# Kernel tuning notes

Hardware: AMD Instinct MI355X
Metric: run time of the kernel (lower is better)

The kernel has to match this reference:

```python
import jax, jax.numpy as jnp
import numpy as np

FEAT = 256
HID = 256
HEADS = 4
DH = HID // HEADS
SCALE = DH ** (-0.5)


def _linear(x, W, b):
    # torch nn.Linear convention: W is [out, in]
    return jnp.einsum('...i,oi->...o', x, W) + b


def _layernorm(x, gamma, beta, eps=1e-5):
    mu = jnp.mean(x, axis=-1, keepdims=True)
    var = jnp.mean(jnp.square(x - mu), axis=-1, keepdims=True)
    return (x - mu) * jax.lax.rsqrt(var + eps) * gamma + beta


def setup_inputs() -> dict:
    key = jax.random.key(0)
    ks = jax.random.split(key, 16)
    B, N = 4, 2048
    def w(k, shape, fan_in):
        return jax.random.uniform(k, shape, jnp.float32, -1.0, 1.0) / np.sqrt(fan_in)
    return {
        'x0': jax.random.normal(ks[0], (B, N, FEAT), jnp.float32),
        'x1': jax.random.normal(ks[1], (B, N, FEAT), jnp.float32),
        'Wqk': w(ks[2], (HID, FEAT), FEAT), 'bqk': w(ks[3], (HID,), FEAT),
        'Wv': w(ks[4], (HID, FEAT), FEAT), 'bv': w(ks[5], (HID,), FEAT),
        'Wp': w(ks[6], (HID, HID), HID), 'bp': w(ks[7], (HID,), HID),
        'W1': w(ks[8], (FEAT * 2, FEAT + HID), FEAT + HID), 'b1': w(ks[9], (FEAT * 2,), FEAT + HID),
        'gamma': jnp.ones((FEAT * 2,), jnp.float32), 'beta': jnp.zeros((FEAT * 2,), jnp.float32),
        'W2': w(ks[10], (FEAT, FEAT * 2), FEAT * 2), 'b2': w(ks[11], (FEAT,), FEAT * 2),
    }


def _forward(x0, x1, Wqk, bqk, Wv, bv, Wp, bp, W1, b1, gamma, beta, W2, b2):
    B, N0, _ = x0.shape
    N1 = x1.shape[1]

    def heads(t):  # [B, N, HID] -> [B, H, N, DH]
        return t.reshape(t.shape[0], t.shape[1], HEADS, DH).transpose(0, 2, 1, 3)

    qk0 = heads(_linear(x0, Wqk, bqk)) * (SCALE ** 0.5)
    qk1 = heads(_linear(x1, Wqk, bqk)) * (SCALE ** 0.5)
    v0 = heads(_linear(x0, Wv, bv))
    v1 = heads(_linear(x1, Wv, bv))

    sim = jnp.einsum('bhid,bhjd->bhij', qk0, qk1)  # [B,H,N0,N1]
    attn01 = jax.nn.softmax(sim, axis=-1)                      # rows over N1
    attn10 = jax.nn.softmax(sim.transpose(0, 1, 3, 2), axis=-1)  # [B,H,N1,N0], rows over N0

    m0 = jnp.einsum('bhij,bhjd->bhid', attn01, v1)  # [B,H,N0,DH]
    m1 = jnp.einsum('bhij,bhjd->bhid', attn10, v0)  # [B,H,N1,DH]

    def merge(t):  # [B,H,N,DH] -> [B,N,HID]
        return t.transpose(0, 2, 1, 3).reshape(t.shape[0], t.shape[2], HID)

    m0 = _linear(merge(m0), Wp, bp)
    m1 = _linear(merge(m1), Wp, bp)

    def mlp(x, m):
        h = _linear(jnp.concatenate([x, m], axis=-1), W1, b1)
        h = jax.nn.gelu(_layernorm(h, gamma, beta), approximate=False)
        return x + _linear(h, W2, b2)

    return mlp(x0, m0), mlp(x1, m1)


def reference(x0, x1, Wqk, bqk, Wv, bv, Wp, bp, W1, b1, gamma, beta, W2, b2):
    return _forward(x0, x1, Wqk, bqk, Wv, bv, Wp, bp, W1, b1, gamma, beta, W2, b2)
```

## Files before the change

### kernel.cpp

```cpp
#include <hip/hip_runtime.h>
#include <hip/hip_bf16.h>
#include <math.h>

typedef __hip_bfloat16 hbf;
typedef __attribute__((ext_vector_type(8))) short short8;
typedef __attribute__((ext_vector_type(4))) short short4v;
typedef __attribute__((ext_vector_type(4))) float f32x4;

#define ROWS 8192
#define SQSL 0.4246609001440095f

__device__ __forceinline__ short f2b(float f) {
    union { hbf h; short s; } u; u.h = __float2bfloat16(f); return u.s;
}
__device__ __forceinline__ float b2f(short s) {
    union { unsigned u; float f; } x;
    x.u = ((unsigned)(unsigned short)s) << 16; return x.f;
}

__global__ __launch_bounds__(256)
void prep(const float* __restrict__ Wqk, const float* __restrict__ Wv,
          const float* __restrict__ Wp, const float* __restrict__ W1,
          const float* __restrict__ W2,
          const float* __restrict__ bp, const float* __restrict__ b1,
          short* __restrict__ wq, short* __restrict__ wv,
          short* __restrict__ w1c, short* __restrict__ w2,
          float* __restrict__ bc)
{
    const int bid = blockIdx.x, tid = threadIdx.x;
    if (bid < 512) {
        const float* src; short* dst; int base; float sc = 1.f;
        if (bid < 64)       { src = Wqk; dst = wq; base = bid;       sc = SQSL; }
        else if (bid < 128) { src = Wv;  dst = wv; base = bid - 64; }
        else if (bid < 384) {
            int i = (bid - 128) * 256 + tid;
            int n = i >> 7, c = (i & 127) * 4;
            if (c < 256) {
                float4 f = ((const float4*)W1)[i];
                short4v s;
                s[0] = f2b(f.x); s[1] = f2b(f.y); s[2] = f2b(f.z); s[3] = f2b(f.w);
                *(short4v*)(w1c + (size_t)n * 512 + c) = s;
            }
            return;
        }
        else                { src = W2;  dst = w2; base = bid - 384; }
        int i = base * 256 + tid;
        float4 f = ((const float4*)src)[i];
        short4v s;
        s[0] = f2b(f.x * sc); s[1] = f2b(f.y * sc);
        s[2] = f2b(f.z * sc); s[3] = f2b(f.w * sc);
        *(short4v*)(dst + (size_t)i * 4) = s;
    } else if (bid < 1024) {
        int n = bid - 512;
        const float* wrow = W1 + (size_t)n * 512 + 256;
        float acc = 0.f;
        for (int k = 0; k < 256; ++k)
            acc += wrow[k] * Wp[(size_t)k * 256 + tid];
        w1c[(size_t)n * 512 + 256 + tid] = f2b(acc);
    } else {
        int n = (bid - 1024) * 256 + tid;
        const float* wrow = W1 + (size_t)n * 512 + 256;
        float acc = b1[n];
        for (int k = 0; k < 256; ++k) acc += wrow[k] * bp[k];
        bc[n] = acc;
    }
}

__global__ __launch_bounds__(256)
void gemm_qkv(const float* __restrict__ x0, const float* __restrict__ x1,
              const short* __restrict__ Wa, const short* __restrict__ Wb,
              const float* __restrict__ bias0, const float* __restrict__ bias1,
              short* __restrict__ qkb, short* __restrict__ vtb)
{
    const int fid  = blockIdx.x + (blockIdx.y << 2);
    const int col0 = (fid >> 8) * 128;
    const int row0 = (fid & 255) * 64;
    const int tid = threadIdx.x;
    const int lane = tid & 63, wave = tid >> 6;
    const int ln = lane & 15, quad = lane >> 4;
    const int wm = wave & 1, wn = wave >> 1;

    __shared__ short smem[64 * 72 + 128 * 72];
    short* As = smem;
    short* Bs = smem + 64 * 72;
    short* Vt = smem;

    const int ar = tid >> 2, ac = tid & 3;

    f32x4 acc[2][4];
    #pragma unroll
    for (int i = 0; i < 2; ++i)
        #pragma unroll
        for (int j = 0; j < 4; ++j) acc[i][j] = {0.f, 0.f, 0.f, 0.f};

    const short* wbase = (col0 < 256) ? Wa + (size_t)col0 * 256
                                      : Wb + (size_t)(col0 - 256) * 256;
    const float* xrow = (row0 + ar < ROWS)
        ? x0 + (size_t)(row0 + ar) * 256
        : x1 + (size_t)(row0 + ar - ROWS) * 256;

    float4 aF[4];
    short8 bR[4];
    #pragma unroll
    for (int i = 0; i < 4; ++i) aF[i] = ((const float4*)(xrow + ac * 16))[i];
    bR[0] = *(const short8*)(wbase + (size_t)ar * 256 + ac * 16);
    bR[1] = *(const short8*)(wbase + (size_t)ar * 256 + ac * 16 + 8);
    bR[2] = *(const short8*)(wbase + (size_t)(ar + 64) * 256 + ac * 16);
    bR[3] = *(const short8*)(wbase + (size_t)(ar + 64) * 256 + ac * 16 + 8);

    for (int k0 = 0; k0 < 256; k0 += 64) {
        {
            short8 s0, s1;
            s0[0] = f2b(aF[0].x); s0[1] = f2b(aF[0].y); s0[2] = f2b(aF[0].z); s0[3] = f2b(aF[0].w);
            s0[4] = f2b(aF[1].x); s0[5] = f2b(aF[1].y); s0[6] = f2b(aF[1].z); s0[7] = f2b(aF[1].w);
            s1[0] = f2b(aF[2].x); s1[1] = f2b(aF[2].y); s1[2] = f2b(aF[2].z); s1[3] = f2b(aF[2].w);
            s1[4] = f2b(aF[3].x); s1[5] = f2b(aF[3].y); s1[6] = f2b(aF[3].z); s1[7] = f2b(aF[3].w);
            *(short8*)&As[ar * 72 + ac * 16]     = s0;
            *(short8*)&As[ar * 72 + ac * 16 + 8] = s1;
        }
        *(short8*)&Bs[ar * 72 + ac * 16]            = bR[0];
        *(short8*)&Bs[ar * 72 + ac * 16 + 8]        = bR[1];
        *(short8*)&Bs[(ar + 64) * 72 + ac * 16]     = bR[2];
        *(short8*)&Bs[(ar + 64) * 72 + ac * 16 + 8] = bR[3];
        __syncthreads();

        if (k0 + 64 < 256) {
            const int kk = k0 + 64 + ac * 16;
            #pragma unroll
            for (int i = 0; i < 4; ++i) aF[i] = ((const float4*)(xrow + kk))[i];
            bR[0] = *(const short8*)(wbase + (size_t)ar * 256 + kk);
            bR[1] = *(const short8*)(wbase + (size_t)ar * 256 + kk + 8);
            bR[2] = *(const short8*)(wbase + (size_t)(ar + 64) * 256 + kk);
            bR[3] = *(const short8*)(wbase + (size_t)(ar + 64) * 256 + kk + 8);
        }

        short8 a[2][2], b[4][2];
        #pragma unroll
        for (int mi = 0; mi < 2; ++mi)
            #pragma unroll
            for (int ks = 0; ks < 2; ++ks)
                a[mi][ks] = *(const short8*)&As[(wm * 32 + mi * 16 + ln) * 72 + ks * 32 + quad * 8];
        #pragma unroll
        for (int nj = 0; nj < 4; ++nj)
            #pragma unroll
            for (int ks = 0; ks < 2; ++ks)
                b[nj][ks] = *(const short8*)&Bs[(wn * 64 + nj * 16 + ln) * 72 + ks * 32 + quad * 8];
        #pragma unroll
        for (int mi = 0; mi < 2; ++mi)
            #pragma unroll
            for (int nj = 0; nj < 4; ++nj) {
                acc[mi][nj] = __builtin_amdgcn_mfma_f32_16x16x32_bf16(
                                  b[nj][0], a[mi][0], acc[mi][nj], 0, 0, 0);
                acc[mi][nj] = __builtin_amdgcn_mfma_f32_16x16x32_bf16(
                                  b[nj][1], a[mi][1], acc[mi][nj], 0, 0, 0);
            }
        __syncthreads();
    }

    if (col0 < 256) {
        #pragma unroll
        for (int nj = 0; nj < 4; ++nj) {
            const int wcol = col0 + wn * 64 + nj * 16 + quad * 4;
            float4 bb = *(const float4*)(bias0 + wcol);
            #pragma unroll
            for (int mi = 0; mi < 2; ++mi) {
                const int tok = row0 + wm * 32 + mi * 16 + ln;
                f32x4 v = acc[mi][nj];
                short4v o;
                o[0] = f2b(fmaf(bb.x, SQSL, v[0]));
                o[1] = f2b(fmaf(bb.y, SQSL, v[1]));
                o[2] = f2b(fmaf(bb.z, SQSL, v[2]));
                o[3] = f2b(fmaf(bb.w, SQSL, v[3]));
                *(short4v*)(qkb + (size_t)tok * 256 + wcol) = o;
            }
        }
    } else {
        #pragma unroll
        for (int nj = 0; nj < 4; ++nj) {
            const int wrel = wn * 64 + nj * 16 + quad * 4;
            float4 bb = *(const float4*)(bias1 + (col0 - 256) + wrel);
            #pragma unroll
            for (int mi = 0; mi < 2; ++mi) {
                const int tl = wm * 32 + mi * 16 + ln;
                f32x4 v = acc[mi][nj];
                Vt[(wrel + 0) * 72 + tl] = f2b(v[0] + bb.x);
                Vt[(wrel + 1) * 72 + tl] = f2b(v[1] + bb.y);
                Vt[(wrel + 2) * 72 + tl] = f2b(v[2] + bb.z);
                Vt[(wrel + 3) * 72 + tl] = f2b(v[3] + bb.w);
            }
        }
        __syncthreads();
        {
            const int g4 = (row0 >> 11) * 4, tc0 = row0 & 2047;
            const int r = tid >> 1, hf = tid & 1;
            const int vcol = (col0 - 256) + r;
            const int hh = vcol >> 6, d = vcol & 63;
            short* dst = vtb + (size_t)((g4 + hh) * 64 + d) * 2048 + tc0 + hf * 32;
            #pragma unroll
            for (int cc = 0; cc < 4; ++cc)
                *(short8*)(dst + cc * 8) = *(const short8*)&Vt[r * 72 + hf * 32 + cc * 8];
        }
    }
}

__global__ __launch_bounds__(128, 2)
void attn8(const short* __restrict__ qkb, const short* __restrict__ vtbuf,
           short* __restrict__ pO0, short* __restrict__ pO1,
           float* __restrict__ l0, float* __restrict__ l1)
{
    const int nfl = blockIdx.x + (blockIdx.y << 4) + (blockIdx.z << 8);
    const int qt  = nfl >> 6;
    const int gg  = nfl & 63;
    const int b    = (gg >> 2) & 3, h = gg & 3;
    const int dir  = gg >> 5;
    const int half = (gg >> 4) & 1;
    const int tid = threadIdx.x;
    const int lane = tid & 63, wave = tid >> 6;
    const int ln   = lane & 15, quad = lane >> 4;

    const int qbase = dir * ROWS + b * 2048;
    const int kbase = (1 - dir) * ROWS + b * 2048;
    const int vg    = ((1 - dir) * 4 + b) * 4 + h;
    const int jlo   = half * 1024, jhi = jlo + 1024;

    short* __restrict__ pO = half ? pO1 : pO0;
    float* __restrict__ lb = half ? l1  : l0;

    __shared__ short QP[128 * 72];
    __shared__ short KS[64 * 72];
    __shared__ short VT[64 * 72];

    const int c = tid & 7, r0 = tid >> 3;
    #pragma unroll
    for (int g = 0; g < 8; ++g) {
        int r = r0 + g * 16;
        *(short8*)&QP[r * 72 + c * 8] =
            *(const short8*)(qkb + (size_t)(qbase + qt * 128 + r) * 256 + h * 64 + c * 8);
    }
    #pragma unroll
    for (int g = 0; g < 4; ++g) {
        int r = r0 + g * 16;
        *(short8*)&KS[r * 72 + c * 8] =
            *(const short8*)(qkb + (size_t)(kbase + jlo + r) * 256 + h * 64 + c * 8);
        *(short8*)&VT[r * 72 + c * 8] =
            *(const short8*)(vtbuf + (size_t)(vg * 64 + r) * 2048 + jlo + c * 8);
    }
    __syncthreads();

    short8 qf[4][2];
    #pragma unroll
    for (int mi = 0; mi < 4; ++mi)
        #pragma unroll
        for (int ks = 0; ks < 2; ++ks)
            qf[mi][ks] = *(const short8*)&QP[(wave * 64 + mi * 16 + ln) * 72
                                             + ks * 32 + quad * 8];

    short8 ones;
    #pragma unroll
    for (int j = 0; j < 8; ++j) ones[j] = (short)0x3F80;

    f32x4 Ot[4][4];
    #pragma unroll
    for (int mi = 0; mi < 4; ++mi)
        #pragma unroll
        for (int dt = 0; dt < 4; ++dt) Ot[mi][dt] = {0.f, 0.f, 0.f, 0.f};
    f32x4 lacc[4];
    #pragma unroll
    for (int mi = 0; mi < 4; ++mi) lacc[mi] = {0.f, 0.f, 0.f, 0.f};

    for (int j0 = jlo; j0 < jhi; j0 += 64) {
        short8 kreg[4], vreg[4];
        const bool more = (j0 + 64) < jhi;
        if (more) {
            #pragma unroll
            for (int g = 0; g < 4; ++g) {
                int r = r0 + g * 16;
                kreg[g] = *(const short8*)(qkb + (size_t)(kbase + j0 + 64 + r) * 256
                                           + h * 64 + c * 8);
                vreg[g] = *(const short8*)(vtbuf + (size_t)(vg * 64 + r) * 2048
                                           + j0 + 64 + c * 8);
            }
        }

        f32x4 St[4][4];
        #pragma unroll
        for (int t = 0; t < 4; ++t) {
            short8 k0 = *(const short8*)&KS[(t * 16 + ln) * 72 + quad * 8];
            short8 k1 = *(const short8*)&KS[(t * 16 + ln) * 72 + 32 + quad * 8];
            #pragma unroll
            for (int mi = 0; mi < 4; ++mi) {
                f32x4 z = {0.f, 0.f, 0.f, 0.f};
                z = __builtin_amdgcn_mfma_f32_16x16x32_bf16(k0, qf[mi][0], z, 0, 0, 0);
                St[mi][t] = __builtin_amdgcn_mfma_f32_16x16x32_bf16(k1, qf[mi][1], z, 0, 0, 0);
            }
        }

        #pragma unroll
        for (int mi = 0; mi < 4; ++mi)
            #pragma unroll
            for (int t = 0; t < 4; ++t) {
                float p0 = __builtin_amdgcn_exp2f(St[mi][t][0]);
                float p1 = __builtin_amdgcn_exp2f(St[mi][t][1]);
                float p2 = __builtin_amdgcn_exp2f(St[mi][t][2]);
                float p3 = __builtin_amdgcn_exp2f(St[mi][t][3]);
                unsigned d0 = __builtin_amdgcn_perm(__float_as_uint(p1),
                                                    __float_as_uint(p0), 0x07060302u);
                unsigned d1 = __builtin_amdgcn_perm(__float_as_uint(p3),
                                                    __float_as_uint(p2), 0x07060302u);
                *(int2*)&QP[(wave * 64 + mi * 16 + ln) * 72 + t * 16 + quad * 4] =
                    make_int2((int)d0, (int)d1);
            }

        short8 pa[4][2];
        #pragma unroll
        for (int mi = 0; mi < 4; ++mi)
            #pragma unroll
            for (int ks = 0; ks < 2; ++ks)
                pa[mi][ks] = *(const short8*)&QP[(wave * 64 + mi * 16 + ln) * 72
                                                 + ks * 32 + quad * 8];
        #pragma unroll
        for (int mi = 0; mi < 4; ++mi) {
            lacc[mi] = __builtin_amdgcn_mfma_f32_16x16x32_bf16(
                           ones, pa[mi][0], lacc[mi], 0, 0, 0);
            lacc[mi] = __builtin_amdgcn_mfma_f32_16x16x32_bf16(
                           ones, pa[mi][1], lacc[mi], 0, 0, 0);
        }
        #pragma unroll
        for (int dt = 0; dt < 4; ++dt) {
            short8 v0 = *(const short8*)&VT[(dt * 16 + ln) * 72 + quad * 8];
            short8 v1 = *(const short8*)&VT[(dt * 16 + ln) * 72 + 32 + quad * 8];
            #pragma unroll
            for (int mi = 0; mi < 4; ++mi) {
                Ot[mi][dt] = __builtin_amdgcn_mfma_f32_16x16x32_bf16(
                                 v0, pa[mi][0], Ot[mi][dt], 0, 0, 0);
                Ot[mi][dt] = __builtin_amdgcn_mfma_f32_16x16x32_bf16(
                                 v1, pa[mi][1], Ot[mi][dt], 0, 0, 0);
            }
        }
        __syncthreads();

        if (more) {
            #pragma unroll
            for (int g = 0; g < 4; ++g) {
                int r = r0 + g * 16;
                *(short8*)&KS[r * 72 + c * 8] = kreg[g];
                *(short8*)&VT[r * 72 + c * 8] = vreg[g];
            }
        }
        __syncthreads();
    }

    #pragma unroll
    for (int mi = 0; mi < 4; ++mi) {
        int tok = qbase + qt * 128 + wave * 64 + mi * 16 + ln;
        if (quad == 0) lb[tok] = lacc[mi][0];
        #pragma unroll
        for (int dt = 0; dt < 4; ++dt) {
            short4v o;
            #pragma unroll
            for (int r = 0; r < 4; ++r) o[r] = f2b(Ot[mi][dt][r]);
            *(short4v*)(pO + (size_t)tok * 256 + h * 64 + dt * 16 + quad * 4) = o;
        }
    }
}

__global__ __launch_bounds__(256)
void mlp_fused(const float* __restrict__ x0, const float* __restrict__ x1,
               const short* __restrict__ pO0, const short* __restrict__ pO1,
               const float* __restrict__ l0, const float* __restrict__ l1,
               const short* __restrict__ w1c, const short* __restrict__ w2,
               const float* __restrict__ bc, const float* __restrict__ gamma,
               const float* __restrict__ beta, const float* __restrict__ b2,
               float* __restrict__ out)
{
    const int tok0 = blockIdx.x * 32;
    const int tid = threadIdx.x;
    const int lane = tid & 63, wave = tid >> 6;
    const int ln = lane & 15, quad = lane >> 4;

    __shared__ short H [32 * 520];
    __shared__ short Bs[256 * 72];
    __shared__ float stats[4][2][32];

    const int br = tid >> 2, bq = tid & 3;
    short8 bp[8];
    auto loadB = [&](const short* W, int rw, int k0) {
        const short* src = W + (size_t)(rw + br) * 512 + k0 + bq * 16;
        #pragma unroll
        for (int q = 0; q < 4; ++q) {
            bp[2 * q]     = *(const short8*)(src + (size_t)q * 64 * 512);
            bp[2 * q + 1] = *(const short8*)(src + (size_t)q * 64 * 512 + 8);
        }
    };
    loadB(w1c, 0, 0);

    {
        const int arow = tid >> 3, ac = tid & 7;
        const int tok = tok0 + arow;
        if (ac < 4) {
            const float* xr = (tok < ROWS ? x0 + (size_t)tok * 256
                                          : x1 + (size_t)(tok - ROWS) * 256) + ac * 64;
            #pragma unroll
            for (int cc = 0; cc < 8; ++cc) {
                float4 f0 = ((const float4*)(xr + cc * 8))[0];
                float4 f1 = ((const float4*)(xr + cc * 8))[1];
                short8 s;
                s[0] = f2b(f0.x); s[1] = f2b(f0.y); s[2] = f2b(f0.z); s[3] = f2b(f0.w);
                s[4] = f2b(f1.x); s[5] = f2b(f1.y); s[6] = f2b(f1.z); s[7] = f2b(f1.w);
                *(short8*)&H[arow * 520 + ac * 64 + cc * 8] = s;
            }
        } else {
            const int vc = (ac - 4) * 64;
            const float inv = __builtin_amdgcn_rcpf(l0[tok] + l1[tok]);
            #pragma unroll
            for (int cc = 0; cc < 8; ++cc) {
                short8 a = *(const short8*)(pO0 + (size_t)tok * 256 + vc + cc * 8);
                short8 b = *(const short8*)(pO1 + (size_t)tok * 256 + vc + cc * 8);
                short8 s;
                #pragma unroll
                for (int j = 0; j < 8; ++j)
                    s[j] = f2b((b2f(a[j]) + b2f(b[j])) * inv);
                *(short8*)&H[arow * 520 + 256 + vc + cc * 8] = s;
            }
        }
    }

    f32x4 acc[2][8];
    #pragma unroll
    for (int i = 0; i < 2; ++i)
        #pragma unroll
        for (int j = 0; j < 8; ++j) acc[i][j] = {0.f, 0.f, 0.f, 0.f};

    __syncthreads();

    for (int k2 = 0; k2 < 8; ++k2) {
        const int k0 = k2 * 64;
        short8 a0[2], a1[2];
        #pragma unroll
        for (int ks = 0; ks < 2; ++ks) {
            a0[ks] = *(const short8*)&H[ln * 520 + k0 + ks * 32 + quad * 8];
            a1[ks] = *(const short8*)&H[(16 + ln) * 520 + k0 + ks * 32 + quad * 8];
        }
        #pragma unroll
        for (int p = 0; p < 2; ++p) {
            #pragma unroll
            for (int q = 0; q < 4; ++q) {
                *(short8*)&Bs[(br + q * 64) * 72 + bq * 16]     = bp[2 * q];
                *(short8*)&Bs[(br + q * 64) * 72 + bq * 16 + 8] = bp[2 * q + 1];
            }
            __syncthreads();
            if (p == 0)          loadB(w1c, 256, k0);
            else if (k2 < 7)     loadB(w1c, 0, k0 + 64);
            #pragma unroll
            for (int nj = 0; nj < 4; ++nj) {
                #pragma unroll
                for (int ks = 0; ks < 2; ++ks) {
                    short8 bf = *(const short8*)&Bs[(wave * 64 + nj * 16 + ln) * 72
                                                    + ks * 32 + quad * 8];
                    acc[0][p * 4 + nj] = __builtin_amdgcn_mfma_f32_16x16x32_bf16(
                                             bf, a0[ks], acc[0][p * 4 + nj], 0, 0, 0);
                    acc[1][p * 4 + nj] = __builtin_amdgcn_mfma_f32_16x16x32_bf16(
                                             bf, a1[ks], acc[1][p * 4 + nj], 0, 0, 0);
                }
            }
            __syncthreads();
        }
    }

    loadB(w2, 0, 0);

    #pragma unroll
    for (int p = 0; p < 2; ++p)
        #pragma unroll
        for (int nj = 0; nj < 4; ++nj) {
            int hcol = p * 256 + wave * 64 + nj * 16 + quad * 4;
            float4 bb = *(const float4*)(bc + hcol);
            acc[0][p * 4 + nj][0] += bb.x; acc[1][p * 4 + nj][0] += bb.x;
            acc[0][p * 4 + nj][1] += bb.y; acc[1][p * 4 + nj][1] += bb.y;
            acc[0][p * 4 + nj][2] += bb.z; acc[1][p * 4 + nj][2] += bb.z;
            acc[0][p * 4 + nj][3] += bb.w; acc[1][p * 4 + nj][3] += bb.w;
        }

    #pragma unroll
    for (int mi = 0; mi < 2; ++mi) {
        float s1 = 0.f, s2 = 0.f;
        #pragma unroll
        for (int j = 0; j < 8; ++j)
            #pragma unroll
            for (int r = 0; r < 4; ++r) {
                float v = acc[mi][j][r];
                s1 += v; s2 += v * v;
            }
        s1 += __shfl_xor(s1, 16); s2 += __shfl_xor(s2, 16);
        s1 += __shfl_xor(s1, 32); s2 += __shfl_xor(s2, 32);
        if (quad == 0) {
            stats[wave][0][mi * 16 + ln] = s1;
            stats[wave][1][mi * 16 + ln] = s2;
        }
    }
    __syncthreads();

    float mean[2], rstd[2];
    #pragma unroll
    for (int mi = 0; mi < 2; ++mi) {
        int t = mi * 16 + ln;
        float s1 = stats[0][0][t] + stats[1][0][t] + stats[2][0][t] + stats[3][0][t];
        float s2 = stats[0][1][t] + stats[1][1][t] + stats[2][1][t] + stats[3][1][t];
        mean[mi] = s1 * (1.f / 512.f);
        float var = s2 * (1.f / 512.f) - mean[mi] * mean[mi];
        rstd[mi] = rsqrtf(var + 1e-5f);
    }

    #pragma unroll
    for (int p = 0; p < 2; ++p)
        #pragma unroll
        for (int nj = 0; nj < 4; ++nj) {
            int hcol = p * 256 + wave * 64 + nj * 16 + quad * 4;
            float4 gm = *(const float4*)(gamma + hcol);
            float4 bt = *(const float4*)(beta + hcol);
            #pragma unroll
            for (int mi = 0; mi < 2; ++mi) {
                short4v o;
                #pragma unroll
                for (int r = 0; r < 4; ++r) {
                    float g = (r == 0) ? gm.x : (r == 1) ? gm.y : (r == 2) ? gm.z : gm.w;
                    float bta = (r == 0) ? bt.x : (r == 1) ? bt.y : (r == 2) ? bt.z : bt.w;
                    float y = (acc[mi][p * 4 + nj][r] - mean[mi]) * rstd[mi] * g + bta;
                    float u = y * fmaf(y * y, 0.0356774081f, 0.7978845608f);
                    float e = __builtin_amdgcn_exp2f(u * -2.8853900818f);
                    o[r] = f2b(y * __builtin_amdgcn_rcpf(1.f + e));
                }
                *(short4v*)&H[(mi * 16 + ln) * 520 + hcol] = o;
            }
        }

    f32x4 acc2[2][4];
    #pragma unroll
    for (int i = 0; i < 2; ++i)
        #pragma unroll
        for (int j = 0; j < 4; ++j) acc2[i][j] = {0.f, 0.f, 0.f, 0.f};

    for (int s = 0; s < 8; ++s) {
        const int k0 = s * 64;
        #pragma unroll
        for (int q = 0; q < 4; ++q) {
            *(short8*)&Bs[(br + q * 64) * 72 + bq * 16]     = bp[2 * q];
            *(short8*)&Bs[(br + q * 64) * 72 + bq * 16 + 8] = bp[2 * q + 1];
        }
        __syncthreads();
        if (s < 7) loadB(w2, 0, k0 + 64);
        short8 h0[2], h1[2];
        #pragma unroll
        for (int ks = 0; ks < 2; ++ks) {
            h0[ks] = *(const short8*)&H[ln * 520 + k0 + ks * 32 + quad * 8];
            h1[ks] = *(const short8*)&H[(16 + ln) * 520 + k0 + ks * 32 + quad * 8];
        }
        #pragma unroll
        for (int nj = 0; nj < 4; ++nj) {
            #pragma unroll
            for (int ks = 0; ks < 2; ++ks) {
                short8 wf = *(const short8*)&Bs[(wave * 64 + nj * 16 + ln) * 72
                                                + ks * 32 + quad * 8];
                acc2[0][nj] = __builtin_amdgcn_mfma_f32_16x16x32_bf16(
                                  wf, h0[ks], acc2[0][nj], 0, 0, 0);
                acc2[1][nj] = __builtin_amdgcn_mfma_f32_16x16x32_bf16(
                                  wf, h1[ks], acc2[1][nj], 0, 0, 0);
            }
        }
        __syncthreads();
    }

    #pragma unroll
    for (int nj = 0; nj < 4; ++nj) {
        int ocol = wave * 64 + nj * 16 + quad * 4;
        float4 bb = *(const float4*)(b2 + ocol);
        #pragma unroll
        for (int mi = 0; mi < 2; ++mi) {
            int tok = tok0 + mi * 16 + ln;
            const float* xr = (tok < ROWS ? x0 + (size_t)tok * 256
                                          : x1 + (size_t)(tok - ROWS) * 256);
            float4 rv = *(const float4*)(xr + ocol);
            float4 o;
            o.x = acc2[mi][nj][0] + bb.x + rv.x;
            o.y = acc2[mi][nj][1] + bb.y + rv.y;
            o.z = acc2[mi][nj][2] + bb.z + rv.z;
            o.w = acc2[mi][nj][3] + bb.w + rv.w;
            *(float4*)(out + (size_t)tok * 256 + ocol) = o;
        }
    }
}

extern "C" void kernel_launch(void* const* d_in, const int* in_sizes, int n_in,
                              void* d_out, int out_size, void* d_ws, size_t ws_size,
                              hipStream_t stream)
{
    const float* x0    = (const float*)d_in[0];
    const float* x1    = (const float*)d_in[1];
    const float* Wqk   = (const float*)d_in[2];
    const float* bqk   = (const float*)d_in[3];
    const float* Wv    = (const float*)d_in[4];
    const float* bv    = (const float*)d_in[5];
    const float* Wp    = (const float*)d_in[6];
    const float* bp    = (const float*)d_in[7];
    const float* W1    = (const float*)d_in[8];
    const float* b1    = (const float*)d_in[9];
    const float* gamma = (const float*)d_in[10];
    const float* beta  = (const float*)d_in[11];
    const float* W2    = (const float*)d_in[12];
    const float* b2    = (const float*)d_in[13];
    float* out = (float*)d_out;

    char* ws = (char*)d_ws;
    const size_t MB = 1024 * 1024;
    short* qkb  = (short*)ws;
    short* vtb  = (short*)(ws + 8  * MB);
    short* pO0  = (short*)(ws + 16 * MB);
    short* pO1  = (short*)(ws + 24 * MB);
    float* l0   = (float*)(ws + 32 * MB);
    float* l1   = l0 + 16384;
    float* bc   = l1 + 16384;
    short* wq   = (short*)(bc + 512);
    short* wv   = wq + 65536;
    short* w1c  = wv + 65536;
    short* w2   = w1c + 262144;

    prep<<<1026, 256, 0, stream>>>(Wqk, Wv, Wp, W1, W2, bp, b1,
                                   wq, wv, w1c, w2, bc);
    gemm_qkv<<<dim3(4, 256), 256, 0, stream>>>(x0, x1, wq, wv, bqk, bv, qkb, vtb);
    attn8<<<dim3(16, 16, 4), 128, 0, stream>>>(qkb, vtb, pO0, pO1, l0, l1);
    mlp_fused<<<512, 256, 0, stream>>>(x0, x1, pO0, pO1, l0, l1, w1c, w2, bc,
                                       gamma, beta, b2, out);
}
```

Before: 196.5 us.

## Overlap MLP weight preparation with QKV GEMM by merging into its grid

```diff
diff --git a/kernel.cpp b/kernel.cpp
--- a/kernel.cpp
+++ b/kernel.cpp
@@ -19,37 +19,43 @@
 }
 
 __global__ __launch_bounds__(256)
-void prep(const float* __restrict__ Wqk, const float* __restrict__ Wv,
-          const float* __restrict__ Wp, const float* __restrict__ W1,
-          const float* __restrict__ W2,
-          const float* __restrict__ bp, const float* __restrict__ b1,
-          short* __restrict__ wq, short* __restrict__ wv,
-          short* __restrict__ w1c, short* __restrict__ w2,
-          float* __restrict__ bc)
+void prep_w(const float* __restrict__ Wqk, const float* __restrict__ Wv,
+            short* __restrict__ wq, short* __restrict__ wv)
 {
     const int bid = blockIdx.x, tid = threadIdx.x;
-    if (bid < 512) {
-        const float* src; short* dst; int base; float sc = 1.f;
-        if (bid < 64)       { src = Wqk; dst = wq; base = bid;       sc = SQSL; }
-        else if (bid < 128) { src = Wv;  dst = wv; base = bid - 64; }
-        else if (bid < 384) {
-            int i = (bid - 128) * 256 + tid;
-            int n = i >> 7, c = (i & 127) * 4;
-            if (c < 256) {
-                float4 f = ((const float4*)W1)[i];
-                short4v s;
-                s[0] = f2b(f.x); s[1] = f2b(f.y); s[2] = f2b(f.z); s[3] = f2b(f.w);
-                *(short4v*)(w1c + (size_t)n * 512 + c) = s;
-            }
-            return;
-        }
-        else                { src = W2;  dst = w2; base = bid - 384; }
-        int i = base * 256 + tid;
-        float4 f = ((const float4*)src)[i];
+    const float* src; short* dst; int base; float sc = 1.f;
+    if (bid < 64) { src = Wqk; dst = wq; base = bid;      sc = SQSL; }
+    else          { src = Wv;  dst = wv; base = bid - 64; }
+    int i = base * 256 + tid;
+    float4 f = ((const float4*)src)[i];
+    short4v s;
+    s[0] = f2b(f.x * sc); s[1] = f2b(f.y * sc);
+    s[2] = f2b(f.z * sc); s[3] = f2b(f.w * sc);
+    *(short4v*)(dst + (size_t)i * 4) = s;
+}
+
+__device__ void prep_big(int bid, int tid,
+                         const float* __restrict__ Wp, const float* __restrict__ W1,
+                         const float* __restrict__ W2, const float* __restrict__ bp,
+                         const float* __restrict__ b1,
+                         short* __restrict__ w1c, short* __restrict__ w2,
+                         float* __restrict__ bc)
+{
+    if (bid < 384) {
+        int i = (bid - 128) * 256 + tid;
+        int n = i >> 7, c = (i & 127) * 4;
+        if (c < 256) {
+            float4 f = ((const float4*)W1)[i];
+            short4v s;
+            s[0] = f2b(f.x); s[1] = f2b(f.y); s[2] = f2b(f.z); s[3] = f2b(f.w);
+            *(short4v*)(w1c + (size_t)n * 512 + c) = s;
+        }
+    } else if (bid < 512) {
+        int i = (bid - 384) * 256 + tid;
+        float4 f = ((const float4*)W2)[i];
         short4v s;
-        s[0] = f2b(f.x * sc); s[1] = f2b(f.y * sc);
-        s[2] = f2b(f.z * sc); s[3] = f2b(f.w * sc);
-        *(short4v*)(dst + (size_t)i * 4) = s;
+        s[0] = f2b(f.x); s[1] = f2b(f.y); s[2] = f2b(f.z); s[3] = f2b(f.w);
+        *(short4v*)(w2 + (size_t)i * 4) = s;
     } else if (bid < 1024) {
         int n = bid - 512;
         const float* wrow = W1 + (size_t)n * 512 + 256;
@@ -70,12 +76,22 @@
 void gemm_qkv(const float* __restrict__ x0, const float* __restrict__ x1,
               const short* __restrict__ Wa, const short* __restrict__ Wb,
               const float* __restrict__ bias0, const float* __restrict__ bias1,
-              short* __restrict__ qkb, short* __restrict__ vtb)
+              short* __restrict__ qkb, short* __restrict__ vtb,
+              const float* __restrict__ Wp, const float* __restrict__ W1,
+              const float* __restrict__ W2f, const float* __restrict__ bpv,
+              const float* __restrict__ b1,
+              short* __restrict__ w1c, short* __restrict__ w2c,
+              float* __restrict__ bc)
 {
-    const int fid  = blockIdx.x + (blockIdx.y << 2);
+    const int bid = blockIdx.x;
+    const int tid = threadIdx.x;
+    if (bid >= 1024) {
+        prep_big(bid - 1024 + 128, tid, Wp, W1, W2f, bpv, b1, w1c, w2c, bc);
+        return;
+    }
+    const int fid  = bid;
     const int col0 = (fid >> 8) * 128;
     const int row0 = (fid & 255) * 64;
-    const int tid = threadIdx.x;
     const int lane = tid & 63, wave = tid >> 6;
     const int ln = lane & 15, quad = lane >> 4;
     const int wm = wave & 1, wn = wave >> 1;
@@ -624,9 +640,9 @@
     short* w1c  = wv + 65536;
     short* w2   = w1c + 262144;
 
-    prep<<<1026, 256, 0, stream>>>(Wqk, Wv, Wp, W1, W2, bp, b1,
-                                   wq, wv, w1c, w2, bc);
-    gemm_qkv<<<dim3(4, 256), 256, 0, stream>>>(x0, x1, wq, wv, bqk, bv, qkb, vtb);
+    prep_w<<<128, 256, 0, stream>>>(Wqk, Wv, wq, wv);
+    gemm_qkv<<<1922, 256, 0, stream>>>(x0, x1, wq, wv, bqk, bv, qkb, vtb,
+                                       Wp, W1, W2, bp, b1, w1c, w2, bc);
     attn8<<<dim3(16, 16, 4), 128, 0, stream>>>(qkb, vtb, pO0, pO1, l0, l1);
     mlp_fused<<<512, 256, 0, stream>>>(x0, x1, pO0, pO1, l0, l1, w1c, w2, bc,
                                        gamma, beta, b2, out);
```

New measurement: 191.4 us, median of 2. 1.03x faster.
